# Kernel tuning notes

Measured on AMD Instinct MI355X. Metric: run time of the kernel, lower is better.

## Reference

```python
import jax, jax.numpy as jnp
import numpy as np

# Dims: M=batch, T=time frames, B=bottleneck channels, H=intermediate channels, KK=kernel size
M, T, B, H, KK = 8, 4000, 128, 512, 3
DILATION = 2
EPS = 1e-8  # gLN eps (ConvTasNet convention)


def prelu(x, a):
    return jnp.where(x >= 0, x, a * x)


def gln(x, gamma, beta):
    # global layer norm over (time, channel) per sample; x: [M, T, C]
    m = jnp.mean(x, axis=(1, 2), keepdims=True)
    v = jnp.mean((x - m) ** 2, axis=(1, 2), keepdims=True)
    return gamma * (x - m) / jnp.sqrt(v + EPS) + beta


def depthwise_conv_same_reflect(x, w):
    # x: [M, C, L], w: [C, K]; dilation 1, 'same' padding with reflect mode
    K = w.shape[1]
    pl = (K - 1) // 2
    xp = jnp.pad(x, ((0, 0), (0, 0), (pl, K - 1 - pl)), mode='reflect')
    return jax.lax.conv_general_dilated(
        xp, w[:, None, :], (1,), 'VALID',
        feature_group_count=x.shape[1], dimension_numbers=('NCH', 'OIH', 'NCH'))


def setup_inputs() -> dict:
    key = jax.random.key(0)
    ks = jax.random.split(key, 12)
    f32 = jnp.float32
    return {
        'x': jax.random.normal(ks[0], (M, T, B), f32),
        'conv1_w': jax.random.normal(ks[1], (H, B), f32) * 0.05,
        'prelu1_a': jnp.asarray(0.25, f32),
        'norm1_g': jnp.ones((H,), f32),
        'norm1_b': jnp.zeros((H,), f32),
        'off_dw_w': jax.random.normal(ks[2], (H, KK), f32) * 0.02,
        'odc_prelu_a': jnp.asarray(0.25, f32),
        'off_pw_w': jax.random.normal(ks[3], (KK, H), f32) * 0.02,
        'opc_prelu_a': jnp.asarray(0.25, f32),
        'dw_w': jax.random.normal(ks[4], (H, KK), f32) * 0.05,
        'dw_b': jax.random.normal(ks[5], (H,), f32) * 0.01,
        'prelu2_a': jnp.asarray(0.25, f32),
        'norm2_g': jnp.ones((H,), f32),
        'norm2_b': jnp.zeros((H,), f32),
        'pw_w': jax.random.normal(ks[6], (B, H), f32) * 0.05,
    }


def reference(x, conv1_w, prelu1_a, norm1_g, norm1_b,
              off_dw_w, odc_prelu_a, off_pw_w, opc_prelu_a,
              dw_w, dw_b, prelu2_a, norm2_g, norm2_b, pw_w):
    dtype = x.dtype
    residual = x
    # 1x1 bottleneck conv -> PReLU -> gLN
    h = jnp.einsum('mtb,hb->mth', x, conv1_w)
    h = gln(prelu(h, prelu1_a), norm1_g, norm1_b)
    hc = jnp.moveaxis(h, 1, 2)  # [M, H, T]

    # --- offset prediction branch (PackedDeformConv1d) ---
    off = depthwise_conv_same_reflect(hc, off_dw_w)          # [M, H, T]
    off = prelu(off, odc_prelu_a)
    off = jnp.einsum('mct,kc->mkt', off, off_pw_w)           # [M, KK, T]
    off = prelu(off, opc_prelu_a)
    offsets = jnp.moveaxis(off, 1, 2)                        # [M, T, KK]

    # --- deformable depthwise conv (same padding, reflect) ---
    pad_tot = DILATION * (KK - 1)
    pl = pad_tot // 2
    xp = jnp.pad(hc, ((0, 0), (0, 0), (pl, pad_tot - pl)), mode='reflect')  # [M,H,Lp]
    Lp = T + pad_tot
    dil_pos = (jnp.arange(KK) * DILATION).astype(dtype)      # [KK]: 0, d, 2d
    t0 = jnp.arange(T, dtype=dtype)[:, None]                 # [T,1]
    Tpos = t0 + dil_pos[None, :] + offsets                   # [M,T,KK]
    Tpos = jnp.clip(Tpos, t0, t0 + dil_pos[-1])              # constrain to receptive field
    U = jnp.clip(jnp.floor(Tpos).astype(jnp.int32), 0, Lp - 2)
    Uf = U.astype(dtype)
    g0 = jax.nn.relu(1.0 - jnp.abs(Uf - Tpos))               # [M,T,KK]
    g1 = jax.nn.relu(1.0 - jnp.abs(Uf + 1.0 - Tpos))
    idx = jnp.broadcast_to(U.reshape(M, 1, T * KK), (M, H, T * KK))
    s0 = jnp.take_along_axis(xp, idx, axis=2).reshape(M, H, T, KK)
    s1 = jnp.take_along_axis(xp, idx + 1, axis=2).reshape(M, H, T, KK)
    sampled = g0[:, None] * s0 + g1[:, None] * s1            # [M,H,T,KK]
    y = jnp.einsum('mhtk,hk->mht', sampled, dw_w) + dw_b[None, :, None]

    # PReLU -> gLN -> 1x1 conv back to B channels, residual add
    y = jnp.moveaxis(y, 1, 2)                                # [M,T,H]
    y = gln(prelu(y, prelu2_a), norm2_g, norm2_b)
    out = jnp.einsum('mth,bh->mtb', y, pw_w)
    return out + residual
```

## Files before the change

kernel.cpp:

```cpp
#include <hip/hip_runtime.h>

#define Mdim 8
#define Tdim 4000
#define Bdim 128
#define Hdim 512
#define NPER (Tdim*Hdim)
#define EPSG 1e-8f

typedef __attribute__((ext_vector_type(8))) short short8;
typedef __attribute__((ext_vector_type(4))) float floatx4;

static __device__ __forceinline__ float bits2f(unsigned short s) {
  union { unsigned int u; float f; } v; v.u = ((unsigned int)s) << 16; return v.f;
}
static __device__ __forceinline__ unsigned short f2bits(float f) {
  union { float f; unsigned int u; } v; v.f = f;
  unsigned int u = v.u;
  u += 0x7fffu + ((u >> 16) & 1u);
  return (unsigned short)(u >> 16);
}
static __device__ __forceinline__ short8 pack8(const float4& a, const float4& b) {
  short8 v;
  v[0]=(short)f2bits(a.x); v[1]=(short)f2bits(a.y); v[2]=(short)f2bits(a.z); v[3]=(short)f2bits(a.w);
  v[4]=(short)f2bits(b.x); v[5]=(short)f2bits(b.y); v[6]=(short)f2bits(b.z); v[7]=(short)f2bits(b.w);
  return v;
}

__global__ __launch_bounds__(256) void k_conv1(
    const float* __restrict__ x,
    const float* __restrict__ w1,
    const float* __restrict__ a1p,
    unsigned short* __restrict__ Hbuf,
    float2* __restrict__ part1)
{
  __shared__ __align__(16) unsigned short ldsW[64*136];
  __shared__ __align__(16) unsigned short ltile[64*72];
  __shared__ float red[512];

  const int tid = threadIdx.x;
  const int t0 = blockIdx.x * 64;
  const int hh = blockIdx.y;
  const int m  = blockIdx.z;

  const int lane = tid & 63, wv = tid >> 6, quad = lane >> 4, l16 = lane & 15;
  int tr = t0 + wv*16 + l16;
  int trc = tr < Tdim ? tr : Tdim-1;
  const float* xrow = x + ((size_t)m*Tdim + trc)*Bdim;
  short8 afr[4];
  #pragma unroll
  for (int ks = 0; ks < 4; ++ks) {
    float4 fa = *(const float4*)&xrow[ks*32 + quad*8];
    float4 fb = *(const float4*)&xrow[ks*32 + quad*8 + 4];
    afr[ks] = pack8(fa, fb);
  }

  const float a1 = a1p[0];
  float lsum = 0.f, lss = 0.f;

  for (int hc = 0; hc < 4; ++hc) {
    const int h0 = (hh*4 + hc) * 64;
    __syncthreads();
    #pragma unroll
    for (int it = 0; it < 4; ++it) {
      int idx = (it*256 + tid) * 8;
      int r = idx >> 7, c = idx & 127;
      float4 fa = *(const float4*)&w1[(size_t)(h0 + r)*Bdim + c];
      float4 fb = *(const float4*)&w1[(size_t)(h0 + r)*Bdim + c + 4];
      *(short8*)&ldsW[r*136 + c] = pack8(fa, fb);
    }
    __syncthreads();

    floatx4 acc[4] = {};
    #pragma unroll
    for (int ks = 0; ks < 4; ++ks) {
      #pragma unroll
      for (int nt = 0; nt < 4; ++nt) {
        short8 bfr = *(const short8*)&ldsW[(nt*16 + l16)*136 + ks*32 + quad*8];
        acc[nt] = __builtin_amdgcn_mfma_f32_16x16x32_bf16(afr[ks], bfr, acc[nt], 0, 0, 0);
      }
    }

    #pragma unroll
    for (int nt = 0; nt < 4; ++nt) {
      int hl = nt*16 + l16;
      #pragma unroll
      for (int r = 0; r < 4; ++r) {
        int tl = wv*16 + quad*4 + r;
        float v = acc[nt][r];
        v = v >= 0.f ? v : a1 * v;
        if (t0 + tl < Tdim) { lsum += v; lss += v*v; }
        ltile[tl*72 + hl] = f2bits(v);
      }
    }
    __syncthreads();
    {
      int tr2 = tid >> 2, ck = (tid & 3) * 16;
      int tg = t0 + tr2;
      if (tg < Tdim) {
        unsigned short* dst = &Hbuf[((size_t)m*Tdim + tg)*Hdim + h0 + ck];
        *(short8*)&dst[0] = *(const short8*)&ltile[tr2*72 + ck];
        *(short8*)&dst[8] = *(const short8*)&ltile[tr2*72 + ck + 8];
      }
    }
  }

  red[tid] = lsum; red[256 + tid] = lss;
  __syncthreads();
  for (int s = 128; s > 0; s >>= 1) {
    if (tid < s) { red[tid] += red[tid + s]; red[256+tid] += red[256+tid+s]; }
    __syncthreads();
  }
  if (tid == 0)
    part1[((size_t)m*2 + hh)*63 + blockIdx.x] = make_float2(red[0], red[256]);
}

__global__ __launch_bounds__(256) void k_deform(
    const unsigned short* __restrict__ Hbuf,
    const float2* __restrict__ part1,
    const float* __restrict__ g1w,
    const float* __restrict__ b1w,
    const float* __restrict__ odw,
    const float* __restrict__ aodcp,
    const float* __restrict__ opw,
    const float* __restrict__ aopcp,
    const float* __restrict__ dww,
    const float* __restrict__ dwb,
    const float* __restrict__ a2p,
    unsigned short* __restrict__ Ybuf,
    float2* __restrict__ part2)
{
  __shared__ float s_stats[2];
  __shared__ float rsum[4], rss[4];
  const int tid = threadIdx.x, lane = tid & 63, w = tid >> 6;
  const int tb = blockIdx.x*8 + w*2;
  const int m = blockIdx.y;
  const int c8 = lane*8;
  const unsigned short* base = Hbuf + (size_t)m*Tdim*Hdim;

  short8 hrow[2][3];
  #pragma unroll
  for (int tt = 0; tt < 2; ++tt) {
    int t = tb + tt;
    int tm1 = (t == 0) ? 1 : t-1;
    int tp1 = (t == Tdim-1) ? Tdim-2 : t+1;
    hrow[tt][0] = *(const short8*)&base[(size_t)tm1*Hdim + c8];
    hrow[tt][1] = *(const short8*)&base[(size_t)t  *Hdim + c8];
    hrow[tt][2] = *(const short8*)&base[(size_t)tp1*Hdim + c8];
  }
  float g1v[8], b1v[8];
  #pragma unroll
  for (int j = 0; j < 8; j += 4) {
    *(float4*)&g1v[j] = *(const float4*)&g1w[c8 + j];
    *(float4*)&b1v[j] = *(const float4*)&b1w[c8 + j];
  }

  if (tid < 64) {
    float s = 0.f, q = 0.f;
    for (int i = lane; i < 126; i += 64) {
      float2 p = part1[(size_t)m*126 + i];
      s += p.x; q += p.y;
    }
    #pragma unroll
    for (int st = 32; st > 0; st >>= 1) { s += __shfl_xor(s, st); q += __shfl_xor(q, st); }
    if (lane == 0) { s_stats[0] = s; s_stats[1] = q; }
  }
  __syncthreads();
  const float invn = 1.0f/(float)NPER;
  const float mean1 = s_stats[0]*invn;
  const float var1  = fmaxf(s_stats[1]*invn - mean1*mean1, 0.f);
  const float inv1  = 1.0f/sqrtf(var1 + EPSG);

  float oa[2][3] = {};
  {
    const float aodc = aodcp[0];
    float wod[24], q0v[8], q1v[8], q2v[8];
    #pragma unroll
    for (int j = 0; j < 8; j += 4) {
      *(float4*)&q0v[j] = *(const float4*)&opw[c8 + j];
      *(float4*)&q1v[j] = *(const float4*)&opw[Hdim + c8 + j];
      *(float4*)&q2v[j] = *(const float4*)&opw[2*Hdim + c8 + j];
    }
    #pragma unroll
    for (int j = 0; j < 24; j += 4)
      *(float4*)&wod[j] = *(const float4*)&odw[c8*3 + j];

    #pragma unroll
    for (int j = 0; j < 8; ++j) {
      float A = g1v[j] * inv1;
      float C = b1v[j] - mean1*A;
      #pragma unroll
      for (int tt = 0; tt < 2; ++tt) {
        float fm = fmaf(A, bits2f((unsigned short)hrow[tt][0][j]), C);
        float fz = fmaf(A, bits2f((unsigned short)hrow[tt][1][j]), C);
        float fp = fmaf(A, bits2f((unsigned short)hrow[tt][2][j]), C);
        float d = fm*wod[j*3+0] + fz*wod[j*3+1] + fp*wod[j*3+2];
        d = d >= 0.f ? d : aodc*d;
        oa[tt][0] = fmaf(d, q0v[j], oa[tt][0]);
        oa[tt][1] = fmaf(d, q1v[j], oa[tt][1]);
        oa[tt][2] = fmaf(d, q2v[j], oa[tt][2]);
      }
    }
    #pragma unroll
    for (int s = 32; s > 0; s >>= 1) {
      #pragma unroll
      for (int tt = 0; tt < 2; ++tt) {
        oa[tt][0] += __shfl_xor(oa[tt][0], s);
        oa[tt][1] += __shfl_xor(oa[tt][1], s);
        oa[tt][2] += __shfl_xor(oa[tt][2], s);
      }
    }
  }

  const float aopc = aopcp[0];
  const float a2   = a2p[0];
  int I0[2][3], I1[2][3]; float G0[2][3], G1[2][3], GS[2][3];
  #pragma unroll
  for (int tt = 0; tt < 2; ++tt) {
    const float tf = (float)(tb + tt);
    #pragma unroll
    for (int k = 0; k < 3; ++k) {
      float off = oa[tt][k];
      off = off >= 0.f ? off : aopc*off;
      float pos = tf + (float)(2*k) + off;
      pos = fminf(fmaxf(pos, tf), tf + 4.0f);
      int U = (int)floorf(pos);
      if (U > Tdim + 2) U = Tdim + 2;
      float Uf = (float)U;
      G0[tt][k] = fmaxf(0.f, 1.f - fabsf(Uf - pos));
      G1[tt][k] = fmaxf(0.f, 1.f - fabsf(Uf + 1.f - pos));
      GS[tt][k] = G0[tt][k] + G1[tt][k];
      int ia = U - 2; ia = ia < 0 ? -ia : ia; if (ia > Tdim-1) ia = 2*(Tdim-1) - ia;
      int ib = U - 1; ib = ib < 0 ? -ib : ib; if (ib > Tdim-1) ib = 2*(Tdim-1) - ib;
      I0[tt][k] = ia; I1[tt][k] = ib;
    }
  }

  short8 s0v[2][3], s1v[2][3];
  #pragma unroll
  for (int tt = 0; tt < 2; ++tt)
    #pragma unroll
    for (int k = 0; k < 3; ++k) {
      s0v[tt][k] = *(const short8*)&base[(size_t)I0[tt][k]*Hdim + c8];
      s1v[tt][k] = *(const short8*)&base[(size_t)I1[tt][k]*Hdim + c8];
    }

  float bv[8], wd[24];
  #pragma unroll
  for (int j = 0; j < 8; j += 4)
    *(float4*)&bv[j] = *(const float4*)&dwb[c8 + j];
  #pragma unroll
  for (int j = 0; j < 24; j += 4)
    *(float4*)&wd[j] = *(const float4*)&dww[c8*3 + j];

  float lsum = 0.f, lss = 0.f;
  short8 yv[2];
  #pragma unroll
  for (int j = 0; j < 8; ++j) {
    float A = g1v[j] * inv1;
    float C = b1v[j] - mean1*A;
    float w0 = wd[j*3+0], w1 = wd[j*3+1], w2 = wd[j*3+2];
    #pragma unroll
    for (int tt = 0; tt < 2; ++tt) {
      float ybase = fmaf(C, w0*GS[tt][0] + w1*GS[tt][1] + w2*GS[tt][2], bv[j]);
      float t0s = fmaf(G1[tt][0], bits2f((unsigned short)s1v[tt][0][j]), G0[tt][0]*bits2f((unsigned short)s0v[tt][0][j]));
      float t1s = fmaf(G1[tt][1], bits2f((unsigned short)s1v[tt][1][j]), G0[tt][1]*bits2f((unsigned short)s0v[tt][1][j]));
      float t2s = fmaf(G1[tt][2], bits2f((unsigned short)s1v[tt][2][j]), G0[tt][2]*bits2f((unsigned short)s0v[tt][2][j]));
      float acc = w0*t0s + w1*t1s + w2*t2s;
      float y = fmaf(A, acc, ybase);
      float p = y >= 0.f ? y : a2*y;
      lsum += p; lss += p*p;
      yv[tt][j] = (short)f2bits(p);
    }
  }
  #pragma unroll
  for (int tt = 0; tt < 2; ++tt)
    *(short8*)&Ybuf[((size_t)m*Tdim + tb + tt)*Hdim + c8] = yv[tt];

  #pragma unroll
  for (int s = 32; s > 0; s >>= 1) {
    lsum += __shfl_xor(lsum, s);
    lss  += __shfl_xor(lss, s);
  }
  if (lane == 0) { rsum[w] = lsum; rss[w] = lss; }
  __syncthreads();
  if (tid == 0)
    part2[(size_t)m*500 + blockIdx.x] =
      make_float2(rsum[0]+rsum[1]+rsum[2]+rsum[3], rss[0]+rss[1]+rss[2]+rss[3]);
}

__global__ __launch_bounds__(64) void k_w2(
    const float2* __restrict__ part2,
    const float* __restrict__ g2w,
    const float* __restrict__ b2w,
    const float* __restrict__ pww,
    unsigned short* __restrict__ W2,
    float* __restrict__ const2)
{
  const int bid = blockIdx.x;
  const int m = bid >> 7, b = bid & 127;
  const int tid = threadIdx.x;

  float s = 0.f, q = 0.f;
  for (int i = tid; i < 500; i += 64) {
    float2 p = part2[(size_t)m*500 + i];
    s += p.x; q += p.y;
  }
  #pragma unroll
  for (int st = 32; st > 0; st >>= 1) { s += __shfl_xor(s, st); q += __shfl_xor(q, st); }

  const float invn = 1.0f/(float)NPER;
  const float mean2 = s*invn;
  const float var2  = fmaxf(q*invn - mean2*mean2, 0.f);
  const float inv2  = 1.0f/sqrtf(var2 + EPSG);

  const int j8 = tid*8;
  float g2v[8], b2v[8], pv[8];
  #pragma unroll
  for (int j = 0; j < 8; j += 4) {
    *(float4*)&g2v[j] = *(const float4*)&g2w[j8 + j];
    *(float4*)&b2v[j] = *(const float4*)&b2w[j8 + j];
    *(float4*)&pv[j]  = *(const float4*)&pww[(size_t)b*Hdim + j8 + j];
  }
  float csum = 0.f;
  short8 wv8;
  #pragma unroll
  for (int j = 0; j < 8; ++j) {
    float A = g2v[j] * inv2;
    float C = b2v[j] - mean2*A;
    csum = fmaf(C, pv[j], csum);
    wv8[j] = (short)f2bits(A*pv[j]);
  }
  *(short8*)&W2[((size_t)m*Bdim + b)*Hdim + j8] = wv8;

  #pragma unroll
  for (int st = 32; st > 0; st >>= 1) csum += __shfl_down(csum, st);
  if (tid == 0) const2[m*Bdim + b] = csum;
}

__global__ __launch_bounds__(256) void k_out(
    const unsigned short* __restrict__ Ybuf,
    const unsigned short* __restrict__ W2,
    const float* __restrict__ const2,
    const float* __restrict__ x,
    float* __restrict__ out)
{
  __shared__ __align__(16) unsigned short ldsW[64*136];
  __shared__ __align__(16) float ltf[64*68];
  const int tid = threadIdx.x;
  const int t0 = blockIdx.x*64;
  const int n0 = blockIdx.y*64;
  const int m  = blockIdx.z;
  const int lane = tid & 63, wv = tid >> 6, quad = lane >> 4, l16 = lane & 15;
  int tr = t0 + wv*16 + l16;
  int trc = tr < Tdim ? tr : Tdim-1;
  const unsigned short* arow = Ybuf + ((size_t)m*Tdim + trc)*Hdim;
  floatx4 acc[4] = {};
  for (int kc = 0; kc < 4; ++kc) {
    __syncthreads();
    #pragma unroll
    for (int it = 0; it < 4; ++it) {
      int idx = (it*256 + tid)*8;
      int r = idx >> 7, c = idx & 127;
      *(short8*)&ldsW[r*136 + c] =
        *(const short8*)&W2[((size_t)m*Bdim + n0 + r)*Hdim + kc*128 + c];
    }
    __syncthreads();
    #pragma unroll
    for (int ks = 0; ks < 4; ++ks) {
      short8 afr = *(const short8*)&arow[kc*128 + ks*32 + quad*8];
      #pragma unroll
      for (int nt = 0; nt < 4; ++nt) {
        short8 bfr = *(const short8*)&ldsW[(nt*16 + l16)*136 + ks*32 + quad*8];
        acc[nt] = __builtin_amdgcn_mfma_f32_16x16x32_bf16(afr, bfr, acc[nt], 0, 0, 0);
      }
    }
  }
  __syncthreads();
  #pragma unroll
  for (int nt = 0; nt < 4; ++nt) {
    int bl = nt*16 + l16;
    float cb = const2[m*Bdim + n0 + bl];
    #pragma unroll
    for (int r = 0; r < 4; ++r) {
      int tl = wv*16 + quad*4 + r;
      ltf[tl*68 + bl] = acc[nt][r] + cb;
    }
  }
  __syncthreads();
  {
    int tr2 = tid >> 2, ck = (tid & 3) * 16;
    int tg = t0 + tr2;
    if (tg < Tdim) {
      const float* xr = &x[((size_t)m*Tdim + tg)*Bdim + n0 + ck];
      float* orow = &out[((size_t)m*Tdim + tg)*Bdim + n0 + ck];
      #pragma unroll
      for (int j = 0; j < 4; ++j) {
        float4 v = *(const float4*)&ltf[tr2*68 + ck + j*4];
        float4 rx = *(const float4*)&xr[j*4];
        v.x += rx.x; v.y += rx.y; v.z += rx.z; v.w += rx.w;
        *(float4*)&orow[j*4] = v;
      }
    }
  }
}

extern "C" void kernel_launch(void* const* d_in, const int* in_sizes, int n_in,
                              void* d_out, int out_size, void* d_ws, size_t ws_size,
                              hipStream_t stream)
{
  (void)in_sizes; (void)n_in; (void)out_size; (void)ws_size;
  const float* x    = (const float*)d_in[0];
  const float* w1   = (const float*)d_in[1];
  const float* a1   = (const float*)d_in[2];
  const float* g1   = (const float*)d_in[3];
  const float* b1   = (const float*)d_in[4];
  const float* odw  = (const float*)d_in[5];
  const float* aodc = (const float*)d_in[6];
  const float* opw  = (const float*)d_in[7];
  const float* aopc = (const float*)d_in[8];
  const float* dww  = (const float*)d_in[9];
  const float* dwb  = (const float*)d_in[10];
  const float* a2   = (const float*)d_in[11];
  const float* g2   = (const float*)d_in[12];
  const float* b2   = (const float*)d_in[13];
  const float* pww  = (const float*)d_in[14];
  float* out = (float*)d_out;

  char* ws = (char*)d_ws;
  const size_t OFF_P1 = 0;
  const size_t OFF_C2 = 8192;
  const size_t OFF_P2 = 12288;
  const size_t OFF_W2 = 44288;
  const size_t OFF_H  = 1092864;
  const size_t OFF_Y  = 33860864;
  float2* part1  = (float2*)(ws + OFF_P1);
  float*  const2 = (float*)(ws + OFF_C2);
  float2* part2  = (float2*)(ws + OFF_P2);
  unsigned short* W2   = (unsigned short*)(ws + OFF_W2);
  unsigned short* Hbuf = (unsigned short*)(ws + OFF_H);
  unsigned short* Ybuf = (unsigned short*)(ws + OFF_Y);

  k_conv1 <<<dim3(63, 2, 8), 256, 0, stream>>>(x, w1, a1, Hbuf, part1);
  k_deform<<<dim3(500, 8), 256, 0, stream>>>(Hbuf, part1, g1, b1, odw, aodc, opw, aopc, dww, dwb, a2, Ybuf, part2);
  k_w2    <<<dim3(1024), 64, 0, stream>>>(part2, g2, b2, pww, W2, const2);
  k_out   <<<dim3(63, 2, 8), 256, 0, stream>>>(Ybuf, W2, const2, x, out);
}
```

Before: 164.1 us.

## Fold gLN2 scale into GEMM epilogue and halve time tiles in conv kernels

Replaces the per-sample W2 kernel, which scaled weights by the gLN2 statistics, with a batch-independent prep kernel that computes gamma*pw weights plus dot products once. The normalization is then applied algebraically in the k_out epilogue (inv2*acc + const) after reducing part2 stats in-block. Time tiles in k_conv1 and k_out shrink from 64 to 32 rows, and the 4 waves are split across row and column halves, which doubles the block count and removes tail guards. The extra block count means more redundant weight loads into LDS per output element.

```diff
diff --git a/kernel.cpp b/kernel.cpp
--- a/kernel.cpp
+++ b/kernel.cpp
@@ -24,6 +24,37 @@
   v[0]=(short)f2bits(a.x); v[1]=(short)f2bits(a.y); v[2]=(short)f2bits(a.z); v[3]=(short)f2bits(a.w);
   v[4]=(short)f2bits(b.x); v[5]=(short)f2bits(b.y); v[6]=(short)f2bits(b.z); v[7]=(short)f2bits(b.w);
   return v;
+}
+
+__global__ __launch_bounds__(64) void k_prep(
+    const float* __restrict__ g2w,
+    const float* __restrict__ b2w,
+    const float* __restrict__ pww,
+    unsigned short* __restrict__ W2raw,
+    float* __restrict__ dotg2,
+    float* __restrict__ dotb2)
+{
+  const int b = blockIdx.x, tid = threadIdx.x;
+  const int j8 = tid*8;
+  float g2v[8], b2v[8], pv[8];
+  #pragma unroll
+  for (int j = 0; j < 8; j += 4) {
+    *(float4*)&g2v[j] = *(const float4*)&g2w[j8 + j];
+    *(float4*)&b2v[j] = *(const float4*)&b2w[j8 + j];
+    *(float4*)&pv[j]  = *(const float4*)&pww[(size_t)b*Hdim + j8 + j];
+  }
+  float dg = 0.f, db = 0.f;
+  short8 wv8;
+  #pragma unroll
+  for (int j = 0; j < 8; ++j) {
+    dg = fmaf(g2v[j], pv[j], dg);
+    db = fmaf(b2v[j], pv[j], db);
+    wv8[j] = (short)f2bits(g2v[j]*pv[j]);
+  }
+  *(short8*)&W2raw[(size_t)b*Hdim + j8] = wv8;
+  #pragma unroll
+  for (int st = 32; st > 0; st >>= 1) { dg += __shfl_xor(dg, st); db += __shfl_xor(db, st); }
+  if (tid == 0) { dotg2[b] = dg; dotb2[b] = db; }
 }
 
 __global__ __launch_bounds__(256) void k_conv1(
@@ -34,18 +65,18 @@
     float2* __restrict__ part1)
 {
   __shared__ __align__(16) unsigned short ldsW[64*136];
-  __shared__ __align__(16) unsigned short ltile[64*72];
+  __shared__ __align__(16) unsigned short ltile[32*72];
   __shared__ float red[512];
 
   const int tid = threadIdx.x;
-  const int t0 = blockIdx.x * 64;
+  const int t0 = blockIdx.x * 32;
   const int hh = blockIdx.y;
   const int m  = blockIdx.z;
 
   const int lane = tid & 63, wv = tid >> 6, quad = lane >> 4, l16 = lane & 15;
-  int tr = t0 + wv*16 + l16;
-  int trc = tr < Tdim ? tr : Tdim-1;
-  const float* xrow = x + ((size_t)m*Tdim + trc)*Bdim;
+  const int rowHalf = wv & 1, nHalf = wv >> 1;
+  const int tr = t0 + rowHalf*16 + l16;
+  const float* xrow = x + ((size_t)m*Tdim + tr)*Bdim;
   short8 afr[4];
   #pragma unroll
   for (int ks = 0; ks < 4; ++ks) {
@@ -58,7 +89,7 @@
   float lsum = 0.f, lss = 0.f;
 
   for (int hc = 0; hc < 4; ++hc) {
-    const int h0 = (hh*4 + hc) * 64;
+    const int h0 = hh*256 + hc*64;
     __syncthreads();
     #pragma unroll
     for (int it = 0; it < 4; ++it) {
@@ -70,37 +101,33 @@
     }
     __syncthreads();
 
-    floatx4 acc[4] = {};
+    floatx4 acc[2] = {};
     #pragma unroll
     for (int ks = 0; ks < 4; ++ks) {
       #pragma unroll
-      for (int nt = 0; nt < 4; ++nt) {
-        short8 bfr = *(const short8*)&ldsW[(nt*16 + l16)*136 + ks*32 + quad*8];
+      for (int nt = 0; nt < 2; ++nt) {
+        short8 bfr = *(const short8*)&ldsW[(nHalf*32 + nt*16 + l16)*136 + ks*32 + quad*8];
         acc[nt] = __builtin_amdgcn_mfma_f32_16x16x32_bf16(afr[ks], bfr, acc[nt], 0, 0, 0);
       }
     }
 
     #pragma unroll
-    for (int nt = 0; nt < 4; ++nt) {
-      int hl = nt*16 + l16;
+    for (int nt = 0; nt < 2; ++nt) {
+      int hl = nHalf*32 + nt*16 + l16;
       #pragma unroll
       for (int r = 0; r < 4; ++r) {
-        int tl = wv*16 + quad*4 + r;
+        int tl = rowHalf*16 + quad*4 + r;
         float v = acc[nt][r];
         v = v >= 0.f ? v : a1 * v;
-        if (t0 + tl < Tdim) { lsum += v; lss += v*v; }
+        lsum += v; lss += v*v;
         ltile[tl*72 + hl] = f2bits(v);
       }
     }
     __syncthreads();
     {
-      int tr2 = tid >> 2, ck = (tid & 3) * 16;
-      int tg = t0 + tr2;
-      if (tg < Tdim) {
-        unsigned short* dst = &Hbuf[((size_t)m*Tdim + tg)*Hdim + h0 + ck];
-        *(short8*)&dst[0] = *(const short8*)&ltile[tr2*72 + ck];
-        *(short8*)&dst[8] = *(const short8*)&ltile[tr2*72 + ck + 8];
-      }
+      int tr2 = tid >> 3, ck = (tid & 7) * 8;
+      unsigned short* dst = &Hbuf[((size_t)m*Tdim + t0 + tr2)*Hdim + h0 + ck];
+      *(short8*)&dst[0] = *(const short8*)&ltile[tr2*72 + ck];
     }
   }
 
@@ -111,7 +138,7 @@
     __syncthreads();
   }
   if (tid == 0)
-    part1[((size_t)m*2 + hh)*63 + blockIdx.x] = make_float2(red[0], red[256]);
+    part1[((size_t)m*2 + hh)*125 + blockIdx.x] = make_float2(red[0], red[256]);
 }
 
 __global__ __launch_bounds__(256) void k_deform(
@@ -156,8 +183,8 @@
 
   if (tid < 64) {
     float s = 0.f, q = 0.f;
-    for (int i = lane; i < 126; i += 64) {
-      float2 p = part1[(size_t)m*126 + i];
+    for (int i = lane; i < 250; i += 64) {
+      float2 p = part1[(size_t)m*250 + i];
       s += p.x; q += p.y;
     }
     #pragma unroll
@@ -288,73 +315,38 @@
       make_float2(rsum[0]+rsum[1]+rsum[2]+rsum[3], rss[0]+rss[1]+rss[2]+rss[3]);
 }
 
-__global__ __launch_bounds__(64) void k_w2(
-    const float2* __restrict__ part2,
-    const float* __restrict__ g2w,
-    const float* __restrict__ b2w,
-    const float* __restrict__ pww,
-    unsigned short* __restrict__ W2,
-    float* __restrict__ const2)
-{
-  const int bid = blockIdx.x;
-  const int m = bid >> 7, b = bid & 127;
-  const int tid = threadIdx.x;
-
-  float s = 0.f, q = 0.f;
-  for (int i = tid; i < 500; i += 64) {
-    float2 p = part2[(size_t)m*500 + i];
-    s += p.x; q += p.y;
-  }
-  #pragma unroll
-  for (int st = 32; st > 0; st >>= 1) { s += __shfl_xor(s, st); q += __shfl_xor(q, st); }
-
-  const float invn = 1.0f/(float)NPER;
-  const float mean2 = s*invn;
-  const float var2  = fmaxf(q*invn - mean2*mean2, 0.f);
-  const float inv2  = 1.0f/sqrtf(var2 + EPSG);
-
-  const int j8 = tid*8;
-  float g2v[8], b2v[8], pv[8];
-  #pragma unroll
-  for (int j = 0; j < 8; j += 4) {
-    *(float4*)&g2v[j] = *(const float4*)&g2w[j8 + j];
-    *(float4*)&b2v[j] = *(const float4*)&b2w[j8 + j];
-    *(float4*)&pv[j]  = *(const float4*)&pww[(size_t)b*Hdim + j8 + j];
-  }
-  float csum = 0.f;
-  short8 wv8;
-  #pragma unroll
-  for (int j = 0; j < 8; ++j) {
-    float A = g2v[j] * inv2;
-    float C = b2v[j] - mean2*A;
-    csum = fmaf(C, pv[j], csum);
-    wv8[j] = (short)f2bits(A*pv[j]);
-  }
-  *(short8*)&W2[((size_t)m*Bdim + b)*Hdim + j8] = wv8;
-
-  #pragma unroll
-  for (int st = 32; st > 0; st >>= 1) csum += __shfl_down(csum, st);
-  if (tid == 0) const2[m*Bdim + b] = csum;
-}
-
 __global__ __launch_bounds__(256) void k_out(
     const unsigned short* __restrict__ Ybuf,
-    const unsigned short* __restrict__ W2,
-    const float* __restrict__ const2,
+    const unsigned short* __restrict__ W2raw,
+    const float2* __restrict__ part2,
+    const float* __restrict__ dotg2,
+    const float* __restrict__ dotb2,
     const float* __restrict__ x,
     float* __restrict__ out)
 {
   __shared__ __align__(16) unsigned short ldsW[64*136];
-  __shared__ __align__(16) float ltf[64*68];
+  __shared__ __align__(16) float ltf[32*68];
+  __shared__ float s_stats[2];
   const int tid = threadIdx.x;
-  const int t0 = blockIdx.x*64;
+  const int t0 = blockIdx.x*32;
   const int n0 = blockIdx.y*64;
   const int m  = blockIdx.z;
   const int lane = tid & 63, wv = tid >> 6, quad = lane >> 4, l16 = lane & 15;
-  int tr = t0 + wv*16 + l16;
-  int trc = tr < Tdim ? tr : Tdim-1;
-  const unsigned short* arow = Ybuf + ((size_t)m*Tdim + trc)*Hdim;
-  floatx4 acc[4] = {};
+  const int rowHalf = wv & 1, nHalf = wv >> 1;
+
+  if (tid < 64) {
+    float s = 0.f, q = 0.f;
+    for (int i = lane; i < 500; i += 64) {
+      float2 p = part2[(size_t)m*500 + i];
+      s += p.x; q += p.y;
+    }
+    #pragma unroll
+    for (int st = 32; st > 0; st >>= 1) { s += __shfl_xor(s, st); q += __shfl_xor(q, st); }
+    if (lane == 0) { s_stats[0] = s; s_stats[1] = q; }
+  }
+
+  const unsigned short* arow = Ybuf + ((size_t)m*Tdim + t0 + rowHalf*16 + l16)*Hdim;
+  floatx4 acc[2] = {};
   for (int kc = 0; kc < 4; ++kc) {
     __syncthreads();
     #pragma unroll
@@ -362,44 +354,48 @@
       int idx = (it*256 + tid)*8;
       int r = idx >> 7, c = idx & 127;
       *(short8*)&ldsW[r*136 + c] =
-        *(const short8*)&W2[((size_t)m*Bdim + n0 + r)*Hdim + kc*128 + c];
+        *(const short8*)&W2raw[(size_t)(n0 + r)*Hdim + kc*128 + c];
     }
     __syncthreads();
     #pragma unroll
     for (int ks = 0; ks < 4; ++ks) {
       short8 afr = *(const short8*)&arow[kc*128 + ks*32 + quad*8];
       #pragma unroll
-      for (int nt = 0; nt < 4; ++nt) {
-        short8 bfr = *(const short8*)&ldsW[(nt*16 + l16)*136 + ks*32 + quad*8];
+      for (int nt = 0; nt < 2; ++nt) {
+        short8 bfr = *(const short8*)&ldsW[(nHalf*32 + nt*16 + l16)*136 + ks*32 + quad*8];
         acc[nt] = __builtin_amdgcn_mfma_f32_16x16x32_bf16(afr, bfr, acc[nt], 0, 0, 0);
       }
     }
   }
+
+  const float invn = 1.0f/(float)NPER;
+  const float mean2 = s_stats[0]*invn;
+  const float var2  = fmaxf(s_stats[1]*invn - mean2*mean2, 0.f);
+  const float inv2  = 1.0f/sqrtf(var2 + EPSG);
+
   __syncthreads();
   #pragma unroll
-  for (int nt = 0; nt < 4; ++nt) {
-    int bl = nt*16 + l16;
-    float cb = const2[m*Bdim + n0 + bl];
+  for (int nt = 0; nt < 2; ++nt) {
+    int bl = nHalf*32 + nt*16 + l16;
+    int b = n0 + bl;
+    float cst = dotb2[b] - mean2*inv2*dotg2[b];
     #pragma unroll
     for (int r = 0; r < 4; ++r) {
-      int tl = wv*16 + quad*4 + r;
-      ltf[tl*68 + bl] = acc[nt][r] + cb;
+      int tl = rowHalf*16 + quad*4 + r;
+      ltf[tl*68 + bl] = fmaf(inv2, acc[nt][r], cst);
     }
   }
   __syncthreads();
   {
-    int tr2 = tid >> 2, ck = (tid & 3) * 16;
-    int tg = t0 + tr2;
-    if (tg < Tdim) {
-      const float* xr = &x[((size_t)m*Tdim + tg)*Bdim + n0 + ck];
-      float* orow = &out[((size_t)m*Tdim + tg)*Bdim + n0 + ck];
-      #pragma unroll
-      for (int j = 0; j < 4; ++j) {
-        float4 v = *(const float4*)&ltf[tr2*68 + ck + j*4];
-        float4 rx = *(const float4*)&xr[j*4];
-        v.x += rx.x; v.y += rx.y; v.z += rx.z; v.w += rx.w;
-        *(float4*)&orow[j*4] = v;
-      }
+    int tr2 = tid >> 3, ck = (tid & 7) * 8;
+    const float* xr = &x[((size_t)m*Tdim + t0 + tr2)*Bdim + n0 + ck];
+    float* orow = &out[((size_t)m*Tdim + t0 + tr2)*Bdim + n0 + ck];
+    #pragma unroll
+    for (int j = 0; j < 2; ++j) {
+      float4 v = *(const float4*)&ltf[tr2*68 + ck + j*4];
+      float4 rx = *(const float4*)&xr[j*4];
+      v.x += rx.x; v.y += rx.y; v.z += rx.z; v.w += rx.w;
+      *(float4*)&orow[j*4] = v;
     }
   }
 }
@@ -428,20 +424,22 @@
 
   char* ws = (char*)d_ws;
   const size_t OFF_P1 = 0;
-  const size_t OFF_C2 = 8192;
-  const size_t OFF_P2 = 12288;
-  const size_t OFF_W2 = 44288;
-  const size_t OFF_H  = 1092864;
-  const size_t OFF_Y  = 33860864;
+  const size_t OFF_P2 = 16384;
+  const size_t OFF_DG = 49152;
+  const size_t OFF_DB = 49664;
+  const size_t OFF_WR = 50176;
+  const size_t OFF_H  = 181248;
+  const size_t OFF_Y  = 32949248;
   float2* part1  = (float2*)(ws + OFF_P1);
-  float*  const2 = (float*)(ws + OFF_C2);
   float2* part2  = (float2*)(ws + OFF_P2);
-  unsigned short* W2   = (unsigned short*)(ws + OFF_W2);
-  unsigned short* Hbuf = (unsigned short*)(ws + OFF_H);
-  unsigned short* Ybuf = (unsigned short*)(ws + OFF_Y);
-
-  k_conv1 <<<dim3(63, 2, 8), 256, 0, stream>>>(x, w1, a1, Hbuf, part1);
+  float*  dotg2  = (float*)(ws + OFF_DG);
+  float*  dotb2  = (float*)(ws + OFF_DB);
+  unsigned short* W2raw = (unsigned short*)(ws + OFF_WR);
+  unsigned short* Hbuf  = (unsigned short*)(ws + OFF_H);
+  unsigned short* Ybuf  = (unsigned short*)(ws + OFF_Y);
+
+  k_prep  <<<dim3(128), 64, 0, stream>>>(g2, b2, pww, W2raw, dotg2, dotb2);
+  k_conv1 <<<dim3(125, 2, 8), 256, 0, stream>>>(x, w1, a1, Hbuf, part1);
   k_deform<<<dim3(500, 8), 256, 0, stream>>>(Hbuf, part1, g1, b1, odw, aodc, opw, aopc, dww, dwb, a2, Ybuf, part2);
-  k_w2    <<<dim3(1024), 64, 0, stream>>>(part2, g2, b2, pww, W2, const2);
-  k_out   <<<dim3(63, 2, 8), 256, 0, stream>>>(Ybuf, W2, const2, x, out);
-}
+  k_out   <<<dim3(125, 2, 8), 256, 0, stream>>>(Ybuf, W2raw, part2, dotg2, dotb2, x, out);
+}
```

After: 177.9 us. 8.4% more time.
